# Kernel tuning notes

Hardware: AMD Instinct MI355X
Metric: run time of the kernel (lower is better)

The kernel has to match this reference:

```python
import jax, jax.numpy as jnp
import numpy as np

HEADS = 32
N_KV_HEADS = 8
HEAD_DIM = 128        # n_embd // heads
N_EMBD = 4096
B, T = 2, 2048


def setup_inputs() -> dict:
    key = jax.random.key(0)
    ks = jax.random.split(key, 8)
    x = jax.random.normal(ks[0], (B, T, N_EMBD), jnp.float32)
    # Llama RoPE frequencies: theta = 10000^(-2i/d), angle = pos * theta
    pos = jnp.arange(T, dtype=jnp.float32)
    inv_freq = 1.0 / (10000.0 ** (jnp.arange(0, HEAD_DIM, 2, dtype=jnp.float32) / HEAD_DIM))
    ang = pos[:, None] * inv_freq[None, :]                      # (T, HEAD_DIM//2)
    freq_cos = jnp.cos(ang)
    freq_sin = jnp.sin(ang)
    s = 0.02
    w_q_w = jax.random.normal(ks[1], (HEADS * HEAD_DIM, N_EMBD), jnp.float32) * s
    w_q_b = jax.random.normal(ks[2], (HEADS * HEAD_DIM,), jnp.float32) * s
    w_kv_w = jax.random.normal(ks[3], (2 * N_KV_HEADS * HEAD_DIM, N_EMBD), jnp.float32) * s
    w_kv_b = jax.random.normal(ks[4], (2 * N_KV_HEADS * HEAD_DIM,), jnp.float32) * s
    proj_w = jax.random.normal(ks[5], (N_EMBD, N_EMBD), jnp.float32) * s
    proj_b = jax.random.normal(ks[6], (N_EMBD,), jnp.float32) * s
    return {"x": x, "freq_cos": freq_cos, "freq_sin": freq_sin,
            "w_q_w": w_q_w, "w_q_b": w_q_b, "w_kv_w": w_kv_w, "w_kv_b": w_kv_b,
            "proj_w": proj_w, "proj_b": proj_b, "start_pos": 0}


def _rope(t, cos, sin):
    # t: (B, H, T, HEAD_DIM); complex multiply on interleaved (even, odd) pairs
    tr = t.reshape(t.shape[:-1] + (HEAD_DIM // 2, 2))
    t0, t1 = tr[..., 0], tr[..., 1]
    r0 = t0 * cos - t1 * sin
    r1 = t0 * sin + t1 * cos
    return jnp.stack([r0, r1], axis=-1).reshape(t.shape)


def reference(x, freq_cos, freq_sin, w_q_w, w_q_b, w_kv_w, w_kv_b, proj_w, proj_b, start_pos):
    Bx, Tx, C = x.shape
    g = HEADS // N_KV_HEADS  # GQA group size
    q = (x @ w_q_w.T + w_q_b).reshape(Bx, Tx, HEADS, HEAD_DIM).transpose(0, 2, 1, 3)
    kv = x @ w_kv_w.T + w_kv_b
    k, v = jnp.split(kv, 2, axis=-1)
    k = k.reshape(Bx, Tx, N_KV_HEADS, HEAD_DIM).transpose(0, 2, 1, 3)
    v = v.reshape(Bx, Tx, N_KV_HEADS, HEAD_DIM).transpose(0, 2, 1, 3)
    cos = freq_cos[:Tx]  # (T, HEAD_DIM//2), broadcasts over (B, H)
    sin = freq_sin[:Tx]
    q = _rope(q, cos, sin)
    k = _rope(k, cos, sin)
    # GQA without materializing repeated KV: group query heads per KV head
    qg = q.reshape(Bx, N_KV_HEADS, g, Tx, HEAD_DIM)
    scores = jnp.einsum('bkgqd,bkld->bkgql', qg, k) / jnp.sqrt(jnp.float32(HEAD_DIM))
    causal = jnp.tril(jnp.ones((Tx, Tx), dtype=bool))
    scores = jnp.where(causal, scores, -jnp.inf)
    p = jax.nn.softmax(scores, axis=-1)
    y = jnp.einsum('bkgql,bkld->bkgqd', p, v)
    y = y.reshape(Bx, HEADS, Tx, HEAD_DIM).transpose(0, 2, 1, 3).reshape(Bx, Tx, C)
    return y @ proj_w.T + proj_b
```

## Files before the change

kernel.cpp:

```cpp
#include <hip/hip_runtime.h>
#include <hip/hip_bf16.h>
#include <stdint.h>

typedef __hip_bfloat16 bf16;
typedef __attribute__((ext_vector_type(8))) __bf16 bf16x8;
typedef __attribute__((ext_vector_type(4))) float f32x4;
typedef __attribute__((ext_vector_type(16))) float f32x16;

__device__ __forceinline__ void gld16(void* lds, const void* g) {
  __builtin_amdgcn_global_load_lds(
      (const __attribute__((address_space(1))) void*)(uintptr_t)(g),
      (__attribute__((address_space(3))) void*)(uint32_t)(uintptr_t)(lds),
      16, 0, 0);
}

__device__ __forceinline__ uint16_t f2bf(float f) {
  union { bf16 h; uint16_t u; } x; x.h = __float2bfloat16(f); return x.u;
}
__device__ __forceinline__ float bf2f(uint16_t v) {
  union { uint32_t u; float f; } x; x.u = ((uint32_t)v) << 16; return x.f;
}
__device__ __forceinline__ uint32_t pk2(float lo, float hi) {
  uint32_t r;
  asm("v_cvt_pk_bf16_f32 %0, %1, %2" : "=v"(r) : "v"(lo), "v"(hi));
  return r;
}

__global__ __launch_bounds__(256) void k_cast(const float4* __restrict__ in,
                                              uint2* __restrict__ out, int n4) {
  int i = blockIdx.x * 256 + threadIdx.x;
  if (i >= n4) return;
  float4 v = in[i];
  uint32_t a = ((uint32_t)f2bf(v.y) << 16) | f2bf(v.x);
  uint32_t b = ((uint32_t)f2bf(v.w) << 16) | f2bf(v.z);
  out[i] = make_uint2(a, b);
}

template <int OUT_BF16, int MB64>
__global__ __launch_bounds__(512, 2) void k_gemm256(
    const bf16* __restrict__ A, const bf16* __restrict__ B,
    const float* __restrict__ bias, void* __restrict__ C,
    int M, int N, int K, int gx) {
  constexpr int MPP = MB64 / 2;
  constexpr int MI = MB64 * 2;
  constexpr int ABYTES = MB64 * 8192;
  constexpr int SLOT = ABYTES + 32768;
  __shared__ __align__(16) char lds[2 * SLOT];
  const int tid = threadIdx.x;
  const int lane = tid & 63;
  const int w = tid >> 6;
  const int wm = w >> 2;
  const int wn = w & 3;
  const int lm = lane & 15;
  const int lg = lane >> 4;

  const int nwg = gridDim.x;
  const int cpx = nwg >> 3;
  const int bid0 = blockIdx.x;
  const int bid = (bid0 & 7) * cpx + (bid0 >> 3);
  const int bx = bid % gx;
  const int by = bid / gx;
  const size_t bm = (size_t)by * (MB64 * 64);
  const size_t bn = (size_t)bx * 256;

  const int srow = tid >> 3;
  const int scb = ((tid & 7) * 16) ^ ((srow & 7) << 4);
  const char* asrc[MB64];
  const char* bsrc[4];
#pragma unroll
  for (int j = 0; j < MB64; ++j)
    asrc[j] = (const char*)(A + (bm + j * 64 + srow) * K) + scb;
#pragma unroll
  for (int j = 0; j < 4; ++j)
    bsrc[j] = (const char*)(B + (bn + j * 64 + srow) * K) + scb;
  const int ldst = tid * 16;

  const int colb0 = (lg * 16) ^ ((lm & 7) << 4);
  const int colb1 = colb0 ^ 64;

  f32x4 acc[MI][4];
#pragma unroll
  for (int i = 0; i < MI; ++i)
#pragma unroll
    for (int j = 0; j < 4; ++j) acc[i][j] = (f32x4){0.f, 0.f, 0.f, 0.f};

  const int NT = K >> 6;

  {
    char* la = lds;
    char* lb = lds + ABYTES;
#pragma unroll
    for (int j = 0; j < MB64; ++j) gld16(la + j * 8192 + ldst, asrc[j]);
#pragma unroll
    for (int j = 0; j < 4; ++j) gld16(lb + j * 8192 + ldst, bsrc[j]);
  }
  __syncthreads();

  for (int t = 0; t < NT; ++t) {
    const int slot = t & 1;
    const char* la = lds + slot * SLOT;
    const char* lb = la + ABYTES;

    bf16x8 bfrag[4][2];
#pragma unroll
    for (int ni = 0; ni < 4; ++ni) {
      const int br = wn * 64 + ni * 16 + lm;
      bfrag[ni][0] = *(const bf16x8*)(lb + br * 128 + colb0);
      bfrag[ni][1] = *(const bf16x8*)(lb + br * 128 + colb1);
    }
    bf16x8 afA[MPP][2], afB[MPP][2];
#pragma unroll
    for (int q = 0; q < MPP; ++q) {
      const int ar = wm * (MB64 * 32) + q * 16 + lm;
      afA[q][0] = *(const bf16x8*)(la + ar * 128 + colb0);
      afA[q][1] = *(const bf16x8*)(la + ar * 128 + colb1);
    }

    if (t + 1 < NT) {
      char* na = lds + (slot ^ 1) * SLOT;
      char* nb = na + ABYTES;
      const size_t ko = (size_t)(t + 1) * 128;
#pragma unroll
      for (int j = 0; j < MB64; ++j) gld16(na + j * 8192 + ldst, asrc[j] + ko);
#pragma unroll
      for (int j = 0; j < 4; ++j) gld16(nb + j * 8192 + ldst, bsrc[j] + ko);
    }

#pragma unroll
    for (int p = 0; p < 4; ++p) {
      auto& cur = (p & 1) ? afB : afA;
      auto& nxt = (p & 1) ? afA : afB;
      if (p < 3) {
#pragma unroll
        for (int q = 0; q < MPP; ++q) {
          const int ar = wm * (MB64 * 32) + ((p + 1) * MPP + q) * 16 + lm;
          nxt[q][0] = *(const bf16x8*)(la + ar * 128 + colb0);
          nxt[q][1] = *(const bf16x8*)(la + ar * 128 + colb1);
        }
        if constexpr (MPP == 2)
          asm volatile("s_waitcnt lgkmcnt(4)" ::: "memory");
        else
          asm volatile("s_waitcnt lgkmcnt(2)" ::: "memory");
      } else {
        asm volatile("s_waitcnt lgkmcnt(0)" ::: "memory");
      }
      __builtin_amdgcn_sched_barrier(0);
      __builtin_amdgcn_s_setprio(1);
#pragma unroll
      for (int q = 0; q < MPP; ++q) {
        bf16x8 a0 = cur[q][0], a1 = cur[q][1];
#pragma unroll
        for (int ni = 0; ni < 4; ++ni) {
          acc[p * MPP + q][ni] = __builtin_amdgcn_mfma_f32_16x16x32_bf16(
              a0, bfrag[ni][0], acc[p * MPP + q][ni], 0, 0, 0);
          acc[p * MPP + q][ni] = __builtin_amdgcn_mfma_f32_16x16x32_bf16(
              a1, bfrag[ni][1], acc[p * MPP + q][ni], 0, 0, 0);
        }
      }
      __builtin_amdgcn_s_setprio(0);
    }
    __syncthreads();
  }

#pragma unroll
  for (int ni = 0; ni < 4; ++ni) {
    const size_t col = bn + wn * 64 + ni * 16 + lm;
    const float bv = bias[col];
#pragma unroll
    for (int mi = 0; mi < MI; ++mi) {
#pragma unroll
      for (int r = 0; r < 4; ++r) {
        const size_t row = bm + wm * (MB64 * 32) + mi * 16 + lg * 4 + r;
        const float v = acc[mi][ni][r] + bv;
        if (OUT_BF16)
          ((bf16*)C)[row * N + col] = __float2bfloat16(v);
        else
          ((float*)C)[row * N + col] = v;
      }
    }
  }
}

__global__ __launch_bounds__(256) void k_rope_q(
    const uint32_t* __restrict__ qin, const float* __restrict__ fc,
    const float* __restrict__ fs, uint32_t* __restrict__ qout) {
  const int tid = blockIdx.x * 256 + threadIdx.x;
  const int i = tid & 63;
  const int h = (tid >> 6) & 31;
  const int t = (tid >> 11) & 2047;
  const int b = tid >> 22;
  const uint32_t u = qin[tid];
  const float t0 = bf2f((uint16_t)(u & 0xffff));
  const float t1 = bf2f((uint16_t)(u >> 16));
  const float c = fc[t * 64 + i];
  const float s = fs[t * 64 + i];
  const float r0 = t0 * c - t1 * s;
  const float r1 = t0 * s + t1 * c;
  const uint32_t o = ((uint32_t)f2bf(r1) << 16) | f2bf(r0);
  qout[(((size_t)(b * 32 + h)) * 2048 + t) * 64 + i] = o;
}

__global__ __launch_bounds__(256) void k_rope_k(
    const uint32_t* __restrict__ kvin, const float* __restrict__ fc,
    const float* __restrict__ fs, uint32_t* __restrict__ kout) {
  const int tid = blockIdx.x * 256 + threadIdx.x;
  const int i = tid & 63;
  const int kvh = (tid >> 6) & 7;
  const int t = (tid >> 9) & 2047;
  const int b = tid >> 20;
  const uint32_t u = kvin[((size_t)(b * 2048 + t)) * 1024 + kvh * 64 + i];
  const float t0 = bf2f((uint16_t)(u & 0xffff));
  const float t1 = bf2f((uint16_t)(u >> 16));
  const float c = fc[t * 64 + i];
  const float s = fs[t * 64 + i];
  const float r0 = t0 * c - t1 * s;
  const float r1 = t0 * s + t1 * c;
  const uint32_t o = ((uint32_t)f2bf(r1) << 16) | f2bf(r0);
  kout[(((size_t)(b * 8 + kvh)) * 2048 + t) * 64 + i] = o;
}

__global__ __launch_bounds__(256) void k_vt(const bf16* __restrict__ kv,
                                            bf16* __restrict__ vt) {
  __shared__ __align__(16) bf16 tile[64][130];
  const int bh = blockIdx.y;
  const int b = bh >> 3, kvh = bh & 7;
  const int t0 = blockIdx.x * 64;
  const int tid = threadIdx.x;
  const int d0 = (tid & 15) * 8;
  const int tr = tid >> 4;
#pragma unroll
  for (int j = 0; j < 4; ++j) {
    const int trow = tr + j * 16;
    const bf16* src =
        kv + ((size_t)(b * 2048) + t0 + trow) * 2048 + 1024 + kvh * 128 + d0;
    uint4 v = *(const uint4*)src;
    uint32_t* dst = (uint32_t*)&tile[trow][d0];
    dst[0] = v.x; dst[1] = v.y; dst[2] = v.z; dst[3] = v.w;
  }
  __syncthreads();
  const int d = tid >> 1;
  const int th = (tid & 1) * 32;
  uint4* out = (uint4*)(vt + (((size_t)bh) * 128 + d) * 2048 + t0 + th);
  union { bf16 h; uint16_t u; } cv;
#pragma unroll
  for (int j = 0; j < 4; ++j) {
    uint32_t wds[4];
#pragma unroll
    for (int p = 0; p < 4; ++p) {
      cv.h = tile[th + j * 8 + p * 2][d];
      uint32_t lo = cv.u;
      cv.h = tile[th + j * 8 + p * 2 + 1][d];
      wds[p] = lo | ((uint32_t)cv.u << 16);
    }
    uint4 val; val.x = wds[0]; val.y = wds[1]; val.z = wds[2]; val.w = wds[3];
    out[j] = val;
  }
}

__global__ __launch_bounds__(512) void k_attn(
    const bf16* __restrict__ Q, const bf16* __restrict__ Kr,
    const bf16* __restrict__ Vt, bf16* __restrict__ Y) {
  constexpr int T = 2048;
  __shared__ __align__(16) char lds[65536];
  const int tid = threadIdx.x;
  const int lane = tid & 63;
  const int w = tid >> 6;
  const int l31 = lane & 31;
  const int hi = lane >> 5;

  const int n = blockIdx.x;
  const int qc = 7 - (n >> 6);
  const int bh = n & 63;
  const int b = bh >> 5, h = bh & 31, kvh = h >> 2;

  const int qrow = qc * 256 + w * 32 + l31;
  const int qmaxw = qc * 256 + w * 32 + 31;
  const int NT = qc * 4 + 4;

  const bf16* qptr = Q + (((size_t)(b * 32 + h)) * T + qrow) * 128 + hi * 8;
  bf16x8 qf[8];
#pragma unroll
  for (int kt = 0; kt < 8; ++kt) qf[kt] = *(const bf16x8*)(qptr + kt * 16);

  const char* kg = (const char*)(Kr + ((size_t)(b * 8 + kvh)) * T * 128);
  const char* vg = (const char*)(Vt + ((size_t)(b * 8 + kvh)) * 128 * T);
  const char* ksrc[2];
  const char* vsrc[2];
  int kdst[2], vdst[2];
#pragma unroll
  for (int j = 0; j < 2; ++j) {
    const int o = j * 8192 + tid * 16;
    const int krow = o >> 8, kin = o & 255;
    ksrc[j] = kg + (size_t)krow * 256 + (kin ^ ((krow & 15) << 4));
    kdst[j] = o;
    const int vrow = o >> 7, vin = o & 127;
    vsrc[j] = vg + (size_t)vrow * (T * 2) + (vin ^ ((vrow & 7) << 4));
    vdst[j] = 16384 + o;
  }

  f32x16 oacc[4];
#pragma unroll
  for (int d = 0; d < 4; ++d)
#pragma unroll
    for (int r = 0; r < 16; ++r) oacc[d][r] = 0.f;
  float m = -1e30f, l = 0.f;
  const float c1 = 0.08838834764831845f * 1.44269504089f;

#pragma unroll
  for (int j = 0; j < 2; ++j) {
    gld16(lds + kdst[j], ksrc[j]);
    gld16(lds + vdst[j], vsrc[j]);
  }

  for (int it = 0; it < NT; ++it) {
    const int buf = it & 1;
    __syncthreads();

    if (it + 1 < NT) {
      const int nb = buf ^ 1;
      const size_t ko = (size_t)(it + 1) * 16384;
      const size_t vo = (size_t)(it + 1) * 128;
#pragma unroll
      for (int j = 0; j < 2; ++j) {
        gld16(lds + nb * 32768 + kdst[j], ksrc[j] + ko);
        gld16(lds + nb * 32768 + vdst[j], vsrc[j] + vo);
      }
    }

    const int kt0 = it * 64;
    if (kt0 <= qmaxw) {
      const char* kb = lds + buf * 32768;
      const char* vb = kb + 16384;

      f32x16 s0, s1;
#pragma unroll
      for (int r = 0; r < 16; ++r) { s0[r] = 0.f; s1[r] = 0.f; }
      const int kswz = (l31 & 15) << 4;
#pragma unroll
      for (int kt = 0; kt < 8; ++kt) {
        const int cb = (kt * 32 + hi * 16) ^ kswz;
        bf16x8 kf0 = *(const bf16x8*)(kb + l31 * 256 + cb);
        bf16x8 kf1 = *(const bf16x8*)(kb + (32 + l31) * 256 + cb);
        s0 = __builtin_amdgcn_mfma_f32_32x32x16_bf16(kf0, qf[kt], s0, 0, 0, 0);
        s1 = __builtin_amdgcn_mfma_f32_32x32x16_bf16(kf1, qf[kt], s1, 0, 0, 0);
      }

      float tmax = -1e30f;
#pragma unroll
      for (int r = 0; r < 16; ++r) {
        const int key0 = kt0 + (r & 3) + 8 * (r >> 2) + 4 * hi;
        float v0 = s0[r] * c1;
        v0 = (key0 <= qrow) ? v0 : -1e30f;
        s0[r] = v0; tmax = fmaxf(tmax, v0);
        float v1 = s1[r] * c1;
        v1 = (key0 + 32 <= qrow) ? v1 : -1e30f;
        s1[r] = v1; tmax = fmaxf(tmax, v1);
      }
      tmax = fmaxf(tmax, __shfl_xor(tmax, 32));

      const float mn = fmaxf(m, tmax);
      const float alpha = __builtin_amdgcn_exp2f(m - mn);
      m = mn;
      l *= alpha;
      float aw[16];
#pragma unroll
      for (int g = 0; g < 4; ++g)
#pragma unroll
        for (int c = 0; c < 4; ++c)
          aw[g * 4 + c] = __shfl(alpha, g * 8 + hi * 4 + c, 64);
#pragma unroll
      for (int r = 0; r < 16; ++r) {
        const float a2 = aw[(r >> 2) * 4 + (r & 3)];
        oacc[0][r] *= a2; oacc[1][r] *= a2;
        oacc[2][r] *= a2; oacc[3][r] *= a2;
      }

      float ls = 0.f;
#pragma unroll
      for (int r = 0; r < 16; ++r) {
        const float p0 = __builtin_amdgcn_exp2f(s0[r] - m); s0[r] = p0; ls += p0;
        const float p1 = __builtin_amdgcn_exp2f(s1[r] - m); s1[r] = p1; ls += p1;
      }
      l += ls + __shfl_xor(ls, 32);

#pragma unroll
      for (int t = 0; t < 4; ++t) {
        uint32_t a0, a1, b0, b1;
        if (t == 0) {
          a0 = pk2(s0[0], s0[1]); a1 = pk2(s0[2], s0[3]);
          b0 = pk2(s0[4], s0[5]); b1 = pk2(s0[6], s0[7]);
        } else if (t == 1) {
          a0 = pk2(s0[8], s0[9]); a1 = pk2(s0[10], s0[11]);
          b0 = pk2(s0[12], s0[13]); b1 = pk2(s0[14], s0[15]);
        } else if (t == 2) {
          a0 = pk2(s1[0], s1[1]); a1 = pk2(s1[2], s1[3]);
          b0 = pk2(s1[4], s1[5]); b1 = pk2(s1[6], s1[7]);
        } else {
          a0 = pk2(s1[8], s1[9]); a1 = pk2(s1[10], s1[11]);
          b0 = pk2(s1[12], s1[13]); b1 = pk2(s1[14], s1[15]);
        }
        const uint32_t sa0 = __shfl_xor(a0, 32), sa1 = __shfl_xor(a1, 32);
        const uint32_t sb0 = __shfl_xor(b0, 32), sb1 = __shfl_xor(b1, 32);
        union { uint32_t u[4]; bf16x8 v; } A;
        A.u[0] = hi ? sb0 : a0;
        A.u[1] = hi ? sb1 : a1;
        A.u[2] = hi ? b0 : sa0;
        A.u[3] = hi ? b1 : sa1;
#pragma unroll
        for (int d = 0; d < 4; ++d) {
          const int vrow = d * 32 + l31;
          const int vcb = (32 * t + 16 * hi) ^ ((vrow & 7) << 4);
          bf16x8 vf = *(const bf16x8*)(vb + vrow * 128 + vcb);
          oacc[d] = __builtin_amdgcn_mfma_f32_32x32x16_bf16(A.v, vf, oacc[d], 0, 0, 0);
        }
      }
    }
    __syncthreads();
  }

  const float linv = 1.0f / l;
  float lw[16];
#pragma unroll
  for (int g = 0; g < 4; ++g)
#pragma unroll
    for (int c = 0; c < 4; ++c)
      lw[g * 4 + c] = __shfl(linv, g * 8 + hi * 4 + c, 64);
  bf16* yb = Y + ((size_t)b * T) * 4096 + h * 128 + l31;
#pragma unroll
  for (int d = 0; d < 4; ++d)
#pragma unroll
    for (int r = 0; r < 16; ++r) {
      const int qp = (r & 3) + 8 * (r >> 2) + 4 * hi;
      const size_t trow = qc * 256 + w * 32 + qp;
      yb[trow * 4096 + d * 32] =
          __float2bfloat16(oacc[d][r] * lw[(r >> 2) * 4 + (r & 3)]);
    }
}

extern "C" void kernel_launch(void* const* d_in, const int* in_sizes, int n_in,
                              void* d_out, int out_size, void* d_ws, size_t ws_size,
                              hipStream_t stream) {
  const float* x = (const float*)d_in[0];
  const float* fcos = (const float*)d_in[1];
  const float* fsin = (const float*)d_in[2];
  const float* wq = (const float*)d_in[3];
  const float* bq = (const float*)d_in[4];
  const float* wkv = (const float*)d_in[5];
  const float* bkv = (const float*)d_in[6];
  const float* wp = (const float*)d_in[7];
  const float* bp = (const float*)d_in[8];

  char* ws = (char*)d_ws;
  size_t off = 0;
  auto alloc = [&](size_t bytes) {
    char* p = ws + off;
    off += (bytes + 255) & ~(size_t)255;
    return p;
  };
  bf16* xb = (bf16*)alloc(16777216ull * 2);
  bf16* wqb = (bf16*)alloc(16777216ull * 2);
  bf16* wkvb = (bf16*)alloc(8388608ull * 2);
  bf16* wpb = (bf16*)alloc(16777216ull * 2);
  bf16* qb = (bf16*)alloc(16777216ull * 2);
  bf16* kvb = (bf16*)alloc(8388608ull * 2);
  bf16* qr = (bf16*)alloc(16777216ull * 2);
  bf16* kr = (bf16*)alloc(4194304ull * 2);
  bf16* vt = (bf16*)alloc(4194304ull * 2);
  bf16* yb = qb;

  k_cast<<<16384, 256, 0, stream>>>((const float4*)x, (uint2*)xb, 4194304);
  k_cast<<<16384, 256, 0, stream>>>((const float4*)wq, (uint2*)wqb, 4194304);
  k_cast<<<8192, 256, 0, stream>>>((const float4*)wkv, (uint2*)wkvb, 2097152);
  k_cast<<<16384, 256, 0, stream>>>((const float4*)wp, (uint2*)wpb, 4194304);

  k_gemm256<1, 4><<<256, 512, 0, stream>>>(xb, wqb, bq, qb, 4096, 4096, 4096, 16);
  k_gemm256<1, 2><<<256, 512, 0, stream>>>(xb, wkvb, bkv, kvb, 4096, 2048, 4096, 8);

  k_rope_q<<<32768, 256, 0, stream>>>((const uint32_t*)qb, fcos, fsin, (uint32_t*)qr);
  k_rope_k<<<8192, 256, 0, stream>>>((const uint32_t*)kvb, fcos, fsin, (uint32_t*)kr);
  k_vt<<<dim3(32, 16), 256, 0, stream>>>(kvb, vt);

  k_attn<<<512, 512, 0, stream>>>(qr, kr, vt, yb);

  k_gemm256<0, 4><<<256, 512, 0, stream>>>(yb, wpb, bp, d_out, 4096, 4096, 4096, 16);
}
```

Baseline: 495.9 us.

## Fuse RoPE into QKV GEMM epilogues, lazy softmax rescale, MFMA priority in attention

The separate RoPE kernels for Q and K are removed. RoPE is now applied in the GEMM epilogue, using a lane shuffle to pair even and odd elements and writing head-major layouts directly, which saves two kernel launches and a round trip of Q and K through memory. The attention kernel skips the online-softmax rescale when no row max grows by more than a threshold, and raises wave priority around the MFMA blocks. The lazy rescale lets exponentials exceed 1 within a bounded range, which slightly changes numerics. The epilogue's scattered 4-byte stores may be less coalesced.

```diff
diff --git a/kernel.cpp b/kernel.cpp
--- a/kernel.cpp
+++ b/kernel.cpp
@@ -36,11 +36,12 @@
   out[i] = make_uint2(a, b);
 }
 
-template <int OUT_BF16, int MB64>
+template <int MODE, int MB64>
 __global__ __launch_bounds__(512, 2) void k_gemm256(
     const bf16* __restrict__ A, const bf16* __restrict__ B,
     const float* __restrict__ bias, void* __restrict__ C,
-    int M, int N, int K, int gx) {
+    bf16* __restrict__ KR, const float* __restrict__ fc,
+    const float* __restrict__ fs, int M, int N, int K, int gx) {
   constexpr int MPP = MB64 / 2;
   constexpr int MI = MB64 * 2;
   constexpr int ABYTES = MB64 * 8192;
@@ -164,59 +165,48 @@
 
 #pragma unroll
   for (int ni = 0; ni < 4; ++ni) {
-    const size_t col = bn + wn * 64 + ni * 16 + lm;
+    const int col = (int)bn + wn * 64 + ni * 16 + lm;
     const float bv = bias[col];
 #pragma unroll
     for (int mi = 0; mi < MI; ++mi) {
 #pragma unroll
       for (int r = 0; r < 4; ++r) {
-        const size_t row = bm + wm * (MB64 * 32) + mi * 16 + lg * 4 + r;
+        const int row = (int)bm + wm * (MB64 * 32) + mi * 16 + lg * 4 + r;
         const float v = acc[mi][ni][r] + bv;
-        if (OUT_BF16)
-          ((bf16*)C)[row * N + col] = __float2bfloat16(v);
-        else
-          ((float*)C)[row * N + col] = v;
-      }
-    }
-  }
-}
-
-__global__ __launch_bounds__(256) void k_rope_q(
-    const uint32_t* __restrict__ qin, const float* __restrict__ fc,
-    const float* __restrict__ fs, uint32_t* __restrict__ qout) {
-  const int tid = blockIdx.x * 256 + threadIdx.x;
-  const int i = tid & 63;
-  const int h = (tid >> 6) & 31;
-  const int t = (tid >> 11) & 2047;
-  const int b = tid >> 22;
-  const uint32_t u = qin[tid];
-  const float t0 = bf2f((uint16_t)(u & 0xffff));
-  const float t1 = bf2f((uint16_t)(u >> 16));
-  const float c = fc[t * 64 + i];
-  const float s = fs[t * 64 + i];
-  const float r0 = t0 * c - t1 * s;
-  const float r1 = t0 * s + t1 * c;
-  const uint32_t o = ((uint32_t)f2bf(r1) << 16) | f2bf(r0);
-  qout[(((size_t)(b * 32 + h)) * 2048 + t) * 64 + i] = o;
-}
-
-__global__ __launch_bounds__(256) void k_rope_k(
-    const uint32_t* __restrict__ kvin, const float* __restrict__ fc,
-    const float* __restrict__ fs, uint32_t* __restrict__ kout) {
-  const int tid = blockIdx.x * 256 + threadIdx.x;
-  const int i = tid & 63;
-  const int kvh = (tid >> 6) & 7;
-  const int t = (tid >> 9) & 2047;
-  const int b = tid >> 20;
-  const uint32_t u = kvin[((size_t)(b * 2048 + t)) * 1024 + kvh * 64 + i];
-  const float t0 = bf2f((uint16_t)(u & 0xffff));
-  const float t1 = bf2f((uint16_t)(u >> 16));
-  const float c = fc[t * 64 + i];
-  const float s = fs[t * 64 + i];
-  const float r0 = t0 * c - t1 * s;
-  const float r1 = t0 * s + t1 * c;
-  const uint32_t o = ((uint32_t)f2bf(r1) << 16) | f2bf(r0);
-  kout[(((size_t)(b * 8 + kvh)) * 2048 + t) * 64 + i] = o;
+        if constexpr (MODE == 0) {
+          ((float*)C)[(size_t)row * N + col] = v;
+        } else if constexpr (MODE == 2) {
+          const int tt = row & 2047, b = row >> 11;
+          const int h = col >> 7, d = col & 127, i2 = d >> 1;
+          const float c = fc[tt * 64 + i2];
+          const float s = fs[tt * 64 + i2];
+          const float pv = __shfl_xor(v, 1);
+          const float rv = v * c + ((lm & 1) ? pv * s : -(pv * s));
+          const float pr = __shfl_xor(rv, 1);
+          if (!(lm & 1)) {
+            const uint32_t u = f2bf(rv) | ((uint32_t)f2bf(pr) << 16);
+            ((uint32_t*)C)[(((size_t)(b * 32 + h)) * 2048 + tt) * 64 + i2] = u;
+          }
+        } else {
+          const int tt = row & 2047, b = row >> 11;
+          if (col < 1024) {
+            const int kvh = col >> 7, d = col & 127, i2 = d >> 1;
+            const float c = fc[tt * 64 + i2];
+            const float s = fs[tt * 64 + i2];
+            const float pv = __shfl_xor(v, 1);
+            const float rv = v * c + ((lm & 1) ? pv * s : -(pv * s));
+            const float pr = __shfl_xor(rv, 1);
+            if (!(lm & 1)) {
+              const uint32_t u = f2bf(rv) | ((uint32_t)f2bf(pr) << 16);
+              ((uint32_t*)KR)[(((size_t)(b * 8 + kvh)) * 2048 + tt) * 64 + i2] = u;
+            }
+          } else {
+            ((bf16*)C)[(size_t)row * N + col] = __float2bfloat16(v);
+          }
+        }
+      }
+    }
+  }
 }
 
 __global__ __launch_bounds__(256) void k_vt(const bf16* __restrict__ kv,
@@ -336,6 +326,7 @@
 #pragma unroll
       for (int r = 0; r < 16; ++r) { s0[r] = 0.f; s1[r] = 0.f; }
       const int kswz = (l31 & 15) << 4;
+      __builtin_amdgcn_s_setprio(1);
 #pragma unroll
       for (int kt = 0; kt < 8; ++kt) {
         const int cb = (kt * 32 + hi * 16) ^ kswz;
@@ -344,6 +335,7 @@
         s0 = __builtin_amdgcn_mfma_f32_32x32x16_bf16(kf0, qf[kt], s0, 0, 0, 0);
         s1 = __builtin_amdgcn_mfma_f32_32x32x16_bf16(kf1, qf[kt], s1, 0, 0, 0);
       }
+      __builtin_amdgcn_s_setprio(0);
 
       float tmax = -1e30f;
 #pragma unroll
@@ -358,21 +350,23 @@
       }
       tmax = fmaxf(tmax, __shfl_xor(tmax, 32));
 
-      const float mn = fmaxf(m, tmax);
-      const float alpha = __builtin_amdgcn_exp2f(m - mn);
-      m = mn;
-      l *= alpha;
-      float aw[16];
-#pragma unroll
-      for (int g = 0; g < 4; ++g)
-#pragma unroll
-        for (int c = 0; c < 4; ++c)
-          aw[g * 4 + c] = __shfl(alpha, g * 8 + hi * 4 + c, 64);
-#pragma unroll
-      for (int r = 0; r < 16; ++r) {
-        const float a2 = aw[(r >> 2) * 4 + (r & 3)];
-        oacc[0][r] *= a2; oacc[1][r] *= a2;
-        oacc[2][r] *= a2; oacc[3][r] *= a2;
+      if (!__all(tmax <= m + 11.5f)) {
+        const float mn = fmaxf(m, tmax);
+        const float alpha = __builtin_amdgcn_exp2f(m - mn);
+        m = mn;
+        l *= alpha;
+        float aw[16];
+#pragma unroll
+        for (int g = 0; g < 4; ++g)
+#pragma unroll
+          for (int c = 0; c < 4; ++c)
+            aw[g * 4 + c] = __shfl(alpha, g * 8 + hi * 4 + c, 64);
+#pragma unroll
+        for (int r = 0; r < 16; ++r) {
+          const float a2 = aw[(r >> 2) * 4 + (r & 3)];
+          oacc[0][r] *= a2; oacc[1][r] *= a2;
+          oacc[2][r] *= a2; oacc[3][r] *= a2;
+        }
       }
 
       float ls = 0.f;
@@ -406,6 +400,7 @@
         A.u[1] = hi ? sb1 : a1;
         A.u[2] = hi ? b0 : sa0;
         A.u[3] = hi ? b1 : sa1;
+        __builtin_amdgcn_s_setprio(1);
 #pragma unroll
         for (int d = 0; d < 4; ++d) {
           const int vrow = d * 32 + l31;
@@ -413,6 +408,7 @@
           bf16x8 vf = *(const bf16x8*)(vb + vrow * 128 + vcb);
           oacc[d] = __builtin_amdgcn_mfma_f32_32x32x16_bf16(A.v, vf, oacc[d], 0, 0, 0);
         }
+        __builtin_amdgcn_s_setprio(0);
       }
     }
     __syncthreads();
@@ -466,21 +462,21 @@
   bf16* qr = (bf16*)alloc(16777216ull * 2);
   bf16* kr = (bf16*)alloc(4194304ull * 2);
   bf16* vt = (bf16*)alloc(4194304ull * 2);
-  bf16* yb = qb;
 
   k_cast<<<16384, 256, 0, stream>>>((const float4*)x, (uint2*)xb, 4194304);
   k_cast<<<16384, 256, 0, stream>>>((const float4*)wq, (uint2*)wqb, 4194304);
   k_cast<<<8192, 256, 0, stream>>>((const float4*)wkv, (uint2*)wkvb, 2097152);
   k_cast<<<16384, 256, 0, stream>>>((const float4*)wp, (uint2*)wpb, 4194304);
 
-  k_gemm256<1, 4><<<256, 512, 0, stream>>>(xb, wqb, bq, qb, 4096, 4096, 4096, 16);
-  k_gemm256<1, 2><<<256, 512, 0, stream>>>(xb, wkvb, bkv, kvb, 4096, 2048, 4096, 8);
-
-  k_rope_q<<<32768, 256, 0, stream>>>((const uint32_t*)qb, fcos, fsin, (uint32_t*)qr);
-  k_rope_k<<<8192, 256, 0, stream>>>((const uint32_t*)kvb, fcos, fsin, (uint32_t*)kr);
+  k_gemm256<2, 4><<<256, 512, 0, stream>>>(xb, wqb, bq, qr, nullptr, fcos,
+                                           fsin, 4096, 4096, 4096, 16);
+  k_gemm256<3, 2><<<256, 512, 0, stream>>>(xb, wkvb, bkv, kvb, kr, fcos,
+                                           fsin, 4096, 2048, 4096, 8);
+
   k_vt<<<dim3(32, 16), 256, 0, stream>>>(kvb, vt);
 
-  k_attn<<<512, 512, 0, stream>>>(qr, kr, vt, yb);
-
-  k_gemm256<0, 4><<<256, 512, 0, stream>>>(yb, wpb, bp, d_out, 4096, 4096, 4096, 16);
-}
+  k_attn<<<512, 512, 0, stream>>>(qr, kr, vt, qb);
+
+  k_gemm256<0, 4><<<256, 512, 0, stream>>>(qb, wpb, bp, d_out, nullptr,
+                                           nullptr, nullptr, 4096, 4096, 4096, 16);
+}
```

After: 512.0 us. +3.2%, slower.

## Fuse cast kernels, add MFMA priority hints, skip small softmax rescales

Applied to the files above, without the earlier changes.

Merges the four separate fp32-to-bf16 cast launches into one kernel that picks its source and destination by thread index, removing three launch overheads. Raises wave priority around the QK and PV MFMA loops with s_setprio. In attention it skips the running-max update and output rescale when every lane's new tile max is within 11.5 (log2 units) of the current max. This is a lazy-rescale trick that saves multiplies and shuffles but lets exponentials grow up to about 2^11.5, which costs some precision headroom.

```diff
diff --git a/kernel.cpp b/kernel.cpp
--- a/kernel.cpp
+++ b/kernel.cpp
@@ -26,14 +26,23 @@
   return r;
 }
 
-__global__ __launch_bounds__(256) void k_cast(const float4* __restrict__ in,
-                                              uint2* __restrict__ out, int n4) {
+__global__ __launch_bounds__(256) void k_cast4(
+    const float4* __restrict__ x, const float4* __restrict__ wq,
+    const float4* __restrict__ wkv, const float4* __restrict__ wp,
+    uint2* __restrict__ xb, uint2* __restrict__ wqb,
+    uint2* __restrict__ wkvb, uint2* __restrict__ wpb) {
   int i = blockIdx.x * 256 + threadIdx.x;
-  if (i >= n4) return;
-  float4 v = in[i];
+  const float4* src;
+  uint2* dst;
+  int o;
+  if (i < 4194304) { src = x; dst = xb; o = i; }
+  else if (i < 8388608) { src = wq; dst = wqb; o = i - 4194304; }
+  else if (i < 10485760) { src = wkv; dst = wkvb; o = i - 8388608; }
+  else { src = wp; dst = wpb; o = i - 10485760; }
+  float4 v = src[o];
   uint32_t a = ((uint32_t)f2bf(v.y) << 16) | f2bf(v.x);
   uint32_t b = ((uint32_t)f2bf(v.w) << 16) | f2bf(v.z);
-  out[i] = make_uint2(a, b);
+  dst[o] = make_uint2(a, b);
 }
 
 template <int OUT_BF16, int MB64>
@@ -336,6 +345,7 @@
 #pragma unroll
       for (int r = 0; r < 16; ++r) { s0[r] = 0.f; s1[r] = 0.f; }
       const int kswz = (l31 & 15) << 4;
+      __builtin_amdgcn_s_setprio(1);
 #pragma unroll
       for (int kt = 0; kt < 8; ++kt) {
         const int cb = (kt * 32 + hi * 16) ^ kswz;
@@ -344,6 +354,7 @@
         s0 = __builtin_amdgcn_mfma_f32_32x32x16_bf16(kf0, qf[kt], s0, 0, 0, 0);
         s1 = __builtin_amdgcn_mfma_f32_32x32x16_bf16(kf1, qf[kt], s1, 0, 0, 0);
       }
+      __builtin_amdgcn_s_setprio(0);
 
       float tmax = -1e30f;
 #pragma unroll
@@ -358,21 +369,23 @@
       }
       tmax = fmaxf(tmax, __shfl_xor(tmax, 32));
 
-      const float mn = fmaxf(m, tmax);
-      const float alpha = __builtin_amdgcn_exp2f(m - mn);
-      m = mn;
-      l *= alpha;
-      float aw[16];
-#pragma unroll
-      for (int g = 0; g < 4; ++g)
-#pragma unroll
-        for (int c = 0; c < 4; ++c)
-          aw[g * 4 + c] = __shfl(alpha, g * 8 + hi * 4 + c, 64);
-#pragma unroll
-      for (int r = 0; r < 16; ++r) {
-        const float a2 = aw[(r >> 2) * 4 + (r & 3)];
-        oacc[0][r] *= a2; oacc[1][r] *= a2;
-        oacc[2][r] *= a2; oacc[3][r] *= a2;
+      if (!__all(tmax <= m + 11.5f)) {
+        const float mn = fmaxf(m, tmax);
+        const float alpha = __builtin_amdgcn_exp2f(m - mn);
+        m = mn;
+        l *= alpha;
+        float aw[16];
+#pragma unroll
+        for (int g = 0; g < 4; ++g)
+#pragma unroll
+          for (int c = 0; c < 4; ++c)
+            aw[g * 4 + c] = __shfl(alpha, g * 8 + hi * 4 + c, 64);
+#pragma unroll
+        for (int r = 0; r < 16; ++r) {
+          const float a2 = aw[(r >> 2) * 4 + (r & 3)];
+          oacc[0][r] *= a2; oacc[1][r] *= a2;
+          oacc[2][r] *= a2; oacc[3][r] *= a2;
+        }
       }
 
       float ls = 0.f;
@@ -406,6 +419,7 @@
         A.u[1] = hi ? sb1 : a1;
         A.u[2] = hi ? b0 : sa0;
         A.u[3] = hi ? b1 : sa1;
+        __builtin_amdgcn_s_setprio(1);
 #pragma unroll
         for (int d = 0; d < 4; ++d) {
           const int vrow = d * 32 + l31;
@@ -413,6 +427,7 @@
           bf16x8 vf = *(const bf16x8*)(vb + vrow * 128 + vcb);
           oacc[d] = __builtin_amdgcn_mfma_f32_32x32x16_bf16(A.v, vf, oacc[d], 0, 0, 0);
         }
+        __builtin_amdgcn_s_setprio(0);
       }
     }
     __syncthreads();
@@ -468,10 +483,10 @@
   bf16* vt = (bf16*)alloc(4194304ull * 2);
   bf16* yb = qb;
 
-  k_cast<<<16384, 256, 0, stream>>>((const float4*)x, (uint2*)xb, 4194304);
-  k_cast<<<16384, 256, 0, stream>>>((const float4*)wq, (uint2*)wqb, 4194304);
-  k_cast<<<8192, 256, 0, stream>>>((const float4*)wkv, (uint2*)wkvb, 2097152);
-  k_cast<<<16384, 256, 0, stream>>>((const float4*)wp, (uint2*)wpb, 4194304);
+  k_cast4<<<57344, 256, 0, stream>>>((const float4*)x, (const float4*)wq,
+                                     (const float4*)wkv, (const float4*)wp,
+                                     (uint2*)xb, (uint2*)wqb, (uint2*)wkvb,
+                                     (uint2*)wpb);
 
   k_gemm256<1, 4><<<256, 512, 0, stream>>>(xb, wqb, bq, qb, 4096, 4096, 4096, 16);
   k_gemm256<1, 2><<<256, 512, 0, stream>>>(xb, wkvb, bkv, kvb, 4096, 2048, 4096, 8);
```

Result: faster. 477.6 us (-3.7%).
